# Kernel tuning notes

Measured on AMD Instinct MI355X. Metric: run time of the kernel, lower is better.

The kernel has to match this reference:

```python
import jax, jax.numpy as jnp
import numpy as np

B, T = 512, 200
N_SKILLS, M, DK, DV, H = 1000, 50, 64, 64, 128


def setup_inputs() -> dict:
    key = jax.random.key(0)
    ks = jax.random.split(key, 12)
    inp = {
        'skill_seq': jax.random.randint(ks[0], (B, T), 0, N_SKILLS, dtype=jnp.int32),
        'correct_seq': jax.random.randint(ks[1], (B, T), 0, 2, dtype=jnp.int32),
        'mask': jnp.ones((B, T), dtype=jnp.float32),
        'skill_embed': jax.random.normal(ks[2], (N_SKILLS, DK), dtype=jnp.float32),
        'key_memory': jax.random.normal(ks[3], (M, DK), dtype=jnp.float32) * 0.1,
        'value_init': jnp.zeros((M, DV), dtype=jnp.float32),
        'interaction_embed': jax.random.normal(ks[4], (2 * N_SKILLS, DV), dtype=jnp.float32),
        'erase_W': jax.random.normal(ks[5], (DV, DV), dtype=jnp.float32) * 0.05,
        'erase_b': jnp.zeros((DV,), dtype=jnp.float32),
        'add_W': jax.random.normal(ks[6], (DV, DV), dtype=jnp.float32) * 0.05,
        'add_b': jnp.zeros((DV,), dtype=jnp.float32),
        'fc1_W': jax.random.normal(ks[7], (DK + DV, H), dtype=jnp.float32) * 0.05,
        'fc1_b': jnp.zeros((H,), dtype=jnp.float32),
        'fc2_W': jax.random.normal(ks[8], (H, 1), dtype=jnp.float32) * 0.05,
        'fc2_b': jnp.zeros((1,), dtype=jnp.float32),
    }
    return inp


def reference(skill_seq, correct_seq, mask, skill_embed, key_memory, value_init,
              interaction_embed, erase_W, erase_b, add_W, add_b,
              fc1_W, fc1_b, fc2_W, fc2_b):
    n_skills = skill_embed.shape[0]
    b = skill_seq.shape[0]
    # Time-invariant-per-step quantities are precomputed vectorized over (B,T):
    q = skill_embed[skill_seq]                                   # (B,T,dk)
    w = jax.nn.softmax(jnp.einsum('btk,mk->btm', q, key_memory), axis=-1)  # (B,T,M)
    v = interaction_embed[skill_seq + correct_seq * n_skills]    # (B,T,dv)
    e = jax.nn.sigmoid(v @ erase_W + erase_b)                    # (B,T,dv)
    a = jnp.tanh(v @ add_W + add_b)                              # (B,T,dv)

    def step(mem, inputs):
        # mem: (B,M,dv); read BEFORE write, matching the torch loop
        w_t, e_t, a_t = inputs                                   # (B,M),(B,dv),(B,dv)
        read = jnp.einsum('bm,bmv->bv', w_t, mem)                # (B,dv)
        we = w_t[:, :, None]                                     # (B,M,1)
        mem = mem * (1.0 - we * e_t[:, None, :]) + we * a_t[:, None, :]
        return mem, read

    mem0 = jnp.broadcast_to(value_init, (b,) + value_init.shape)
    _, reads = jax.lax.scan(step, mem0,
                            (jnp.swapaxes(w, 0, 1), jnp.swapaxes(e, 0, 1), jnp.swapaxes(a, 0, 1)))
    reads = jnp.swapaxes(reads, 0, 1)                            # (B,T,dv)

    x = jnp.concatenate([q, reads], axis=-1)                     # (B,T,dk+dv)
    h = jax.nn.relu(x @ fc1_W + fc1_b)
    logit = (h @ fc2_W + fc2_b)[..., 0]
    p = jax.nn.sigmoid(logit)
    return p * mask, correct_seq.astype(jnp.float32) * mask
```

## Files before the change

kernel.cpp:

```cpp
#include <hip/hip_runtime.h>
#include <hip/hip_bf16.h>

#define B_  512
#define T_  200
#define NS  1000
#define M_  50
#define DK  64
#define DV  64
#define H_  128
#define NPOS (B_ * T_)

typedef __hip_bfloat16 bf16;
typedef unsigned short ushort_t;
typedef __bf16 bf16x8 __attribute__((ext_vector_type(8)));
typedef float  f32x4  __attribute__((ext_vector_type(4)));

__device__ __forceinline__ float ldf(const void* p, int i, int isbf) {
    return isbf ? __bfloat162float(((const bf16*)p)[i]) : ((const float*)p)[i];
}
__device__ __forceinline__ int sniff(const void* mask) {
    return (*(const unsigned*)mask == 0x3F800000u) ? 0 : 1;
}
__device__ __forceinline__ float rl(float x, int l) {
    return __int_as_float(__builtin_amdgcn_readlane(__float_as_int(x), l));
}
__device__ __forceinline__ ushort_t f2bf(float v) {
    bf16 h = __float2bfloat16(v);
    return *(ushort_t*)&h;
}

__global__ __launch_bounds__(256) void dk27_tabs(
    const void* __restrict__ mask,
    const void* __restrict__ skill_embed, const void* __restrict__ key_memory,
    const void* __restrict__ inter,
    const void* __restrict__ eW, const void* __restrict__ eb,
    const void* __restrict__ aW, const void* __restrict__ ab,
    const void* __restrict__ fc1W, const void* __restrict__ fc1b,
    float* __restrict__ w_tab, unsigned* __restrict__ ea_tab,
    float* __restrict__ hq2, ushort_t* __restrict__ W2f) {
    int isbf = sniff(mask);
    int lane = threadIdx.x & 63;
    int gwid = (blockIdx.x << 2) | (threadIdx.x >> 6);

    if (gwid < NS) {
        int s = gwid;
        float q = ldf(skill_embed, s * DK + lane, isbf);
        float acc = 0.f;
        if (lane < M_) {
            #pragma unroll 16
            for (int k = 0; k < DK; ++k)
                acc = fmaf(rl(q, k), ldf(key_memory, lane * DK + k, isbf), acc);
        }
        float val = (lane < M_) ? acc : -1e30f;
        float mx = val;
        #pragma unroll
        for (int off = 1; off < 64; off <<= 1) mx = fmaxf(mx, __shfl_xor(mx, off, 64));
        float ex = (lane < M_) ? __expf(val - mx) : 0.f;
        float sm = ex;
        #pragma unroll
        for (int off = 1; off < 64; off <<= 1) sm += __shfl_xor(sm, off, 64);
        w_tab[s * 64 + lane] = (lane < M_) ? ex / sm : 0.f;
    } else if (gwid < 3 * NS) {
        int r = gwid - NS;
        float vv = ldf(inter, r * DV + lane, isbf);
        float eacc = ldf(eb, lane, isbf);
        float aacc = ldf(ab, lane, isbf);
        #pragma unroll 16
        for (int u = 0; u < DV; ++u) {
            float vu = rl(vv, u);
            eacc = fmaf(vu, ldf(eW, u * DV + lane, isbf), eacc);
            aacc = fmaf(vu, ldf(aW, u * DV + lane, isbf), aacc);
        }
        float ev = 1.f / (1.f + __expf(-eacc));
        float av = tanhf(aacc);
        ea_tab[r * 64 + lane] = ((unsigned)f2bf(av) << 16) | (unsigned)f2bf(ev);
    } else if (gwid < 4 * NS) {
        int s = gwid - 3 * NS;
        float q = ldf(skill_embed, s * DK + lane, isbf);
        float acc0 = ldf(fc1b, lane, isbf);
        float acc1 = ldf(fc1b, 64 + lane, isbf);
        #pragma unroll 16
        for (int k = 0; k < DK; ++k) {
            float qk = rl(q, k);
            acc0 = fmaf(qk, ldf(fc1W, k * H_ + lane, isbf), acc0);
            acc1 = fmaf(qk, ldf(fc1W, k * H_ + 64 + lane, isbf), acc1);
        }
        hq2[s * H_ + (lane & 15) * 8 +     (lane >> 4)] = acc0;
        hq2[s * H_ + (lane & 15) * 8 + 4 + (lane >> 4)] = acc1;
    } else if (gwid < 4 * NS + 16) {
        int f = gwid - 4 * NS;
        int tile = f >> 1, kk = f & 1;
        int n = tile * 16 + (lane & 15);
        #pragma unroll
        for (int j = 0; j < 8; ++j) {
            int v = kk * 32 + (lane >> 4) * 8 + j;
            W2f[(f * 64 + lane) * 8 + j] = f2bf(ldf(fc1W, (DK + v) * H_ + n, isbf));
        }
    }
}


#define SCROW(W, MEM) \
    acc0 = fmaf(W.x, MEM.x, acc0); \
    acc1 = fmaf(W.y, MEM.y, acc1); \
    acc2 = fmaf(W.z, MEM.z, acc2); \
    acc3 = fmaf(W.w, MEM.w, acc3); \
    MEM.x = fmaf(-W.x, fmaf(e0, MEM.x, -a0), MEM.x); \
    MEM.y = fmaf(-W.y, fmaf(e0, MEM.y, -a0), MEM.y); \
    MEM.z = fmaf(-W.z, fmaf(e0, MEM.z, -a0), MEM.z); \
    MEM.w = fmaf(-W.w, fmaf(e0, MEM.w, -a0), MEM.w);

#define VPTR(P) { size_t u_ = (size_t)(P); asm volatile("" : "+v"(u_)); \
                  (P) = (const f32x4*)u_; }

#define REFILL(ST, S, C) { \
    const f32x4* p_ = (const f32x4*)w_tab + (S) * 16 + 4 * k; \
    VPTR(p_) \
    w##ST##0 = p_[0]; w##ST##1 = p_[1]; w##ST##2 = p_[2]; w##ST##3 = p_[3]; \
    ea##ST = ea_tab[((S) + (C) * NS) * 64 + lane]; }

#define STEP(ST, TP) { \
    float e0 = __uint_as_float(ea##ST << 16); \
    float a0 = __uint_as_float(ea##ST & 0xFFFF0000u); \
    float acc0 = 0.f, acc1 = 0.f, acc2 = 0.f, acc3 = 0.f; \
    SCROW(w##ST##0, mem[0]) SCROW(w##ST##1, mem[1]) \
    SCROW(w##ST##2, mem[2]) SCROW(w##ST##3, mem[3]) \
    read_bf[outb + (TP) * 256] = f2bf((acc0 + acc1) + (acc2 + acc3)); \
    REFILL(ST, curS[TP], curC[TP]) }

__global__ __launch_bounds__(64, 2) void dk27_scan(
    const int*  __restrict__ ss, const int* __restrict__ cs,
    const void* __restrict__ mask, const void* __restrict__ value_init,
    const float* __restrict__ w_tab, const unsigned* __restrict__ ea_tab,
    ushort_t* __restrict__ read_bf) {

    int isbf = sniff(mask);
    int lane = threadIdx.x;
    int bk   = blockIdx.x;
    int b    = bk >> 2, k = bk & 3;
    const int base = b * T_;

    float4 mem[4];
    #pragma unroll
    for (int i = 0; i < 4; ++i) {
        int r = 16 * k + 4 * i;
        mem[i].x = (r + 0 < M_) ? ldf(value_init, (r + 0) * DV + lane, isbf) : 0.f;
        mem[i].y = (r + 1 < M_) ? ldf(value_init, (r + 1) * DV + lane, isbf) : 0.f;
        mem[i].z = (r + 2 < M_) ? ldf(value_init, (r + 2) * DV + lane, isbf) : 0.f;
        mem[i].w = (r + 3 < M_) ? ldf(value_init, (r + 3) * DV + lane, isbf) : 0.f;
    }

    int curS[8], curC[8], nxtS[8], nxtC[8];
    #pragma unroll
    for (int j = 0; j < 8; ++j) { nxtS[j] = ss[base + 2 + j]; nxtC[j] = cs[base + 2 + j]; }

    f32x4 wA0, wA1, wA2, wA3, wB0, wB1, wB2, wB3;
    unsigned eaA, eaB;
    {
        int s_ = ss[base + 0], c_ = cs[base + 0];
        REFILL(A, s_, c_)
        s_ = ss[base + 1]; c_ = cs[base + 1];
        REFILL(B, s_, c_)
    }

    size_t outb = ((size_t)base * 4 + k) * 64 + lane;

    for (int cc = 0; cc < 25; ++cc) {
        #pragma unroll
        for (int j = 0; j < 8; ++j) { curS[j] = nxtS[j]; curC[j] = nxtC[j]; }
        int tb = 8 * cc + 10;
        #pragma unroll
        for (int j = 0; j < 8; ++j) {
            int tf = tb + j; tf = tf < T_ ? tf : T_ - 1;
            nxtS[j] = ss[base + tf]; nxtC[j] = cs[base + tf];
        }
        STEP(A, 0) STEP(B, 1) STEP(A, 2) STEP(B, 3)
        STEP(A, 4) STEP(B, 5) STEP(A, 6) STEP(B, 7)
        outb += 2048;
    }
}

#define FOR8(X) X(0) X(1) X(2) X(3) X(4) X(5) X(6) X(7)
#define DECL_C(t)  f32x4 c##t = {0.f, 0.f, 0.f, 0.f};
#define LOADB(t) bf16x8 b##t##_0 = B8[(2 * (t)) * 64 + lane], \
                        b##t##_1 = B8[(2 * (t) + 1) * 64 + lane];
#define FCKK(kk, p) { \
    bf16x8 av = A8[col * 32 + (kk) * 4 + quad]; \
    c0 = __builtin_amdgcn_mfma_f32_16x16x32_bf16(av, b0_##p, c0, 0, 0, 0); \
    c1 = __builtin_amdgcn_mfma_f32_16x16x32_bf16(av, b1_##p, c1, 0, 0, 0); \
    c2 = __builtin_amdgcn_mfma_f32_16x16x32_bf16(av, b2_##p, c2, 0, 0, 0); \
    c3 = __builtin_amdgcn_mfma_f32_16x16x32_bf16(av, b3_##p, c3, 0, 0, 0); \
    c4 = __builtin_amdgcn_mfma_f32_16x16x32_bf16(av, b4_##p, c4, 0, 0, 0); \
    c5 = __builtin_amdgcn_mfma_f32_16x16x32_bf16(av, b5_##p, c5, 0, 0, 0); \
    c6 = __builtin_amdgcn_mfma_f32_16x16x32_bf16(av, b6_##p, c6, 0, 0, 0); \
    c7 = __builtin_amdgcn_mfma_f32_16x16x32_bf16(av, b7_##p, c7, 0, 0, 0); }
#define HQ(r, t) (((t) < 4) ? qa##r[(t) & 3] : qb##r[(t) & 3])
#define EPI(t) { \
    float h; \
    h = c##t.x + HQ(0, t); x0 = fmaf(fmaxf(h, 0.f), f2w##t, x0); \
    h = c##t.y + HQ(1, t); x1 = fmaf(fmaxf(h, 0.f), f2w##t, x1); \
    h = c##t.z + HQ(2, t); x2 = fmaf(fmaxf(h, 0.f), f2w##t, x2); \
    h = c##t.w + HQ(3, t); x3 = fmaf(fmaxf(h, 0.f), f2w##t, x3); }

__global__ __launch_bounds__(64)
__attribute__((amdgpu_waves_per_eu(3))) void dk27_fc(
    const int*  __restrict__ skill_seq, const int* __restrict__ correct_seq,
    const void* __restrict__ mask,
    const void* __restrict__ fc2W, const void* __restrict__ fc2b,
    const float* __restrict__ hq2, const ushort_t* __restrict__ W2f,
    const ushort_t* __restrict__ read_bf,
    float* __restrict__ out0, float* __restrict__ out1) {

    int isbf = sniff(mask);
    int lane = threadIdx.x;
    int col  = lane & 15, quad = lane >> 4;

    const bf16x8* B8 = (const bf16x8*)W2f;
    FOR8(LOADB)

    float f2w0 = ldf(fc2W,   0 + col, isbf), f2w1 = ldf(fc2W,  16 + col, isbf);
    float f2w2 = ldf(fc2W,  32 + col, isbf), f2w3 = ldf(fc2W,  48 + col, isbf);
    float f2w4 = ldf(fc2W,  64 + col, isbf), f2w5 = ldf(fc2W,  80 + col, isbf);
    float f2w6 = ldf(fc2W,  96 + col, isbf), f2w7 = ldf(fc2W, 112 + col, isbf);
    float f2b  = ldf(fc2b, 0, isbf);

    for (int pg = blockIdx.x; pg < NPOS / 16; pg += gridDim.x) {
        int p0 = pg * 16;
        const bf16x8* A8 = (const bf16x8*)(read_bf + (size_t)p0 * 256);

        int s0r = skill_seq[p0 + quad * 4 + 0];
        int s1r = skill_seq[p0 + quad * 4 + 1];
        int s2r = skill_seq[p0 + quad * 4 + 2];
        int s3r = skill_seq[p0 + quad * 4 + 3];

        f32x4 qa0 = *(const f32x4*)(hq2 + s0r * H_ + col * 8);
        f32x4 qb0 = *(const f32x4*)(hq2 + s0r * H_ + col * 8 + 4);
        f32x4 qa1 = *(const f32x4*)(hq2 + s1r * H_ + col * 8);
        f32x4 qb1 = *(const f32x4*)(hq2 + s1r * H_ + col * 8 + 4);
        f32x4 qa2 = *(const f32x4*)(hq2 + s2r * H_ + col * 8);
        f32x4 qb2 = *(const f32x4*)(hq2 + s2r * H_ + col * 8 + 4);
        f32x4 qa3 = *(const f32x4*)(hq2 + s3r * H_ + col * 8);
        f32x4 qb3 = *(const f32x4*)(hq2 + s3r * H_ + col * 8 + 4);

        FOR8(DECL_C)
        FCKK(0, 0) FCKK(1, 1) FCKK(2, 0) FCKK(3, 1)
        FCKK(4, 0) FCKK(5, 1) FCKK(6, 0) FCKK(7, 1)

        float x0 = 0.f, x1 = 0.f, x2 = 0.f, x3 = 0.f;
        FOR8(EPI)

        #pragma unroll
        for (int off = 1; off < 16; off <<= 1) {
            x0 += __shfl_xor(x0, off, 64);
            x1 += __shfl_xor(x1, off, 64);
            x2 += __shfl_xor(x2, off, 64);
            x3 += __shfl_xor(x3, off, 64);
        }

        float mk0 = ldf(mask, p0 + quad * 4 + 0, isbf);
        float mk1 = ldf(mask, p0 + quad * 4 + 1, isbf);
        float mk2 = ldf(mask, p0 + quad * 4 + 2, isbf);
        float mk3 = ldf(mask, p0 + quad * 4 + 3, isbf);
        if (col == 0) {
            out0[p0 + quad * 4 + 0] = mk0 / (1.f + __expf(-(x0 + f2b)));
            out0[p0 + quad * 4 + 1] = mk1 / (1.f + __expf(-(x1 + f2b)));
            out0[p0 + quad * 4 + 2] = mk2 / (1.f + __expf(-(x2 + f2b)));
            out0[p0 + quad * 4 + 3] = mk3 / (1.f + __expf(-(x3 + f2b)));
        }
        if (col == 1) {
            out1[p0 + quad * 4 + 0] = (float)correct_seq[p0 + quad * 4 + 0] * mk0;
            out1[p0 + quad * 4 + 1] = (float)correct_seq[p0 + quad * 4 + 1] * mk1;
            out1[p0 + quad * 4 + 2] = (float)correct_seq[p0 + quad * 4 + 2] * mk2;
            out1[p0 + quad * 4 + 3] = (float)correct_seq[p0 + quad * 4 + 3] * mk3;
        }
    }
}

extern "C" void kernel_launch(void* const* d_in, const int* in_sizes, int n_in,
                              void* d_out, int out_size, void* d_ws, size_t ws_size,
                              hipStream_t stream) {
    const int*  skill_seq   = (const int*)d_in[0];
    const int*  correct_seq = (const int*)d_in[1];
    const void* mask        = d_in[2];
    const void* skill_embed = d_in[3];
    const void* key_memory  = d_in[4];
    const void* value_init  = d_in[5];
    const void* inter       = d_in[6];
    const void* erase_W     = d_in[7];
    const void* erase_b     = d_in[8];
    const void* add_W       = d_in[9];
    const void* add_b       = d_in[10];
    const void* fc1_W       = d_in[11];
    const void* fc1_b       = d_in[12];
    const void* fc2_W       = d_in[13];
    const void* fc2_b       = d_in[14];
    float* out = (float*)d_out;

    float*    ws      = (float*)d_ws + 16;
    float*    w_tab   = ws;
    unsigned* ea_tab  = (unsigned*)(ws + 64000);
    float*    hq2     = ws + 192000;
    ushort_t* W2f     = (ushort_t*)(ws + 320000);
    ushort_t* read_bf = (ushort_t*)(ws + 336400);

    dk27_tabs<<<1004, 256, 0, stream>>>(mask, skill_embed, key_memory, inter,
                                        erase_W, erase_b, add_W, add_b,
                                        fc1_W, fc1_b,
                                        w_tab, ea_tab, hq2, W2f);

    dk27_scan<<<B_ * 4, 64, 0, stream>>>(skill_seq, correct_seq, mask, value_init,
                                         w_tab, ea_tab, read_bf);

    dk27_fc<<<3200, 64, 0, stream>>>(skill_seq, correct_seq, mask,
                                     fc2_W, fc2_b, hq2, W2f, read_bf,
                                     out, out + (size_t)NPOS);
}
```

Measured before the change: 197.8 us.

## Precompute combined interaction index and restructure scan prefetch with sched barriers

```diff
diff --git a/kernel.cpp b/kernel.cpp
--- a/kernel.cpp
+++ b/kernel.cpp
@@ -29,7 +29,8 @@
     return *(ushort_t*)&h;
 }
 
-__global__ __launch_bounds__(256) void dk27_tabs(
+__global__ __launch_bounds__(256) void dk28_tabs(
+    const int*  __restrict__ ss, const int* __restrict__ cs,
     const void* __restrict__ mask,
     const void* __restrict__ skill_embed, const void* __restrict__ key_memory,
     const void* __restrict__ inter,
@@ -37,7 +38,8 @@
     const void* __restrict__ aW, const void* __restrict__ ab,
     const void* __restrict__ fc1W, const void* __restrict__ fc1b,
     float* __restrict__ w_tab, unsigned* __restrict__ ea_tab,
-    float* __restrict__ hq2, ushort_t* __restrict__ W2f) {
+    float* __restrict__ hq2, ushort_t* __restrict__ W2f,
+    int* __restrict__ qix) {
     int isbf = sniff(mask);
     int lane = threadIdx.x & 63;
     int gwid = (blockIdx.x << 2) | (threadIdx.x >> 6);
@@ -96,40 +98,74 @@
             int v = kk * 32 + (lane >> 4) * 8 + j;
             W2f[(f * 64 + lane) * 8 + j] = f2bf(ldf(fc1W, (DK + v) * H_ + n, isbf));
         }
+    } else if (gwid < 4 * NS + 16 + 400) {
+        int qp = gwid - (4 * NS + 16);
+        int t0 = qp * 256;
+        #pragma unroll
+        for (int i = 0; i < 4; ++i) {
+            int idx = t0 + i * 64 + lane;
+            qix[idx] = ss[idx] + cs[idx] * NS;
+        }
     }
 }
 
 
-#define SCROW(W, MEM) \
-    acc0 = fmaf(W.x, MEM.x, acc0); \
-    acc1 = fmaf(W.y, MEM.y, acc1); \
-    acc2 = fmaf(W.z, MEM.z, acc2); \
-    acc3 = fmaf(W.w, MEM.w, acc3); \
-    MEM.x = fmaf(-W.x, fmaf(e0, MEM.x, -a0), MEM.x); \
-    MEM.y = fmaf(-W.y, fmaf(e0, MEM.y, -a0), MEM.y); \
-    MEM.z = fmaf(-W.z, fmaf(e0, MEM.z, -a0), MEM.z); \
-    MEM.w = fmaf(-W.w, fmaf(e0, MEM.w, -a0), MEM.w);
-
-#define VPTR(P) { size_t u_ = (size_t)(P); asm volatile("" : "+v"(u_)); \
-                  (P) = (const f32x4*)u_; }
-
-#define REFILL(ST, S, C) { \
-    const f32x4* p_ = (const f32x4*)w_tab + (S) * 16 + 4 * k; \
-    VPTR(p_) \
-    w##ST##0 = p_[0]; w##ST##1 = p_[1]; w##ST##2 = p_[2]; w##ST##3 = p_[3]; \
-    ea##ST = ea_tab[((S) + (C) * NS) * 64 + lane]; }
-
-#define STEP(ST, TP) { \
-    float e0 = __uint_as_float(ea##ST << 16); \
-    float a0 = __uint_as_float(ea##ST & 0xFFFF0000u); \
+#define SB0 __builtin_amdgcn_sched_barrier(0);
+
+#define SCROW1(WV, MM, ACC) \
+    ACC = fmaf(WV, MM, ACC); \
+    MM = fmaf(-(WV), fmaf(e0, MM, -a0), MM);
+
+#define SC_STEP(D, EAR, TP, QR) { \
+    float e0 = __uint_as_float(EAR << 16); \
+    float a0 = __uint_as_float(EAR & 0xFFFF0000u); \
     float acc0 = 0.f, acc1 = 0.f, acc2 = 0.f, acc3 = 0.f; \
-    SCROW(w##ST##0, mem[0]) SCROW(w##ST##1, mem[1]) \
-    SCROW(w##ST##2, mem[2]) SCROW(w##ST##3, mem[3]) \
+    SCROW1(D[0],  mem[0].x, acc0) SCROW1(D[1],  mem[0].y, acc1) \
+    SCROW1(D[2],  mem[0].z, acc2) SCROW1(D[3],  mem[0].w, acc3) \
+    SCROW1(D[4],  mem[1].x, acc0) SCROW1(D[5],  mem[1].y, acc1) \
+    SCROW1(D[6],  mem[1].z, acc2) SCROW1(D[7],  mem[1].w, acc3) \
+    SCROW1(D[8],  mem[2].x, acc0) SCROW1(D[9],  mem[2].y, acc1) \
+    SCROW1(D[10], mem[2].z, acc2) SCROW1(D[11], mem[2].w, acc3) \
+    SCROW1(D[12], mem[3].x, acc0) SCROW1(D[13], mem[3].y, acc1) \
+    SCROW1(D[14], mem[3].z, acc2) SCROW1(D[15], mem[3].w, acc3) \
     read_bf[outb + (TP) * 256] = f2bf((acc0 + acc1) + (acc2 + acc3)); \
-    REFILL(ST, curS[TP], curC[TP]) }
-
-__global__ __launch_bounds__(64, 2) void dk27_scan(
-    const int*  __restrict__ ss, const int* __restrict__ cs,
+    EAR = ea_tab[(unsigned)(QR) * 64 + lane]; \
+}
+
+#define FILL_W(D, Q) { \
+    int s_ = (Q) < NS ? (Q) : (Q) - NS; \
+    const float* wp_ = w_tab + s_ * 64 + 16 * k; \
+    _Pragma("unroll") \
+    for (int z = 0; z < 16; ++z) D[z] = wp_[z]; \
+}
+
+#define LDQ(QF, J, TBN) { \
+    int t_ = (TBN) + (J); t_ = t_ < T_ ? t_ : T_ - 1; \
+    QF[J] = qix[base + t_]; \
+}
+
+#define CHUNK(QC, QF, TBN) { \
+    SC_STEP(wA0, eaA, 0, QC[2]) \
+    SB0 FILL_W(wB0, QC[2]) FILL_W(wB1, QC[3]) \
+        LDQ(QF, 0, TBN) LDQ(QF, 1, TBN) SB0 \
+    SC_STEP(wA1, eaB, 1, QC[3]) \
+    SC_STEP(wB0, eaA, 2, QC[4]) \
+    SB0 FILL_W(wA0, QC[4]) FILL_W(wA1, QC[5]) \
+        LDQ(QF, 2, TBN) LDQ(QF, 3, TBN) SB0 \
+    SC_STEP(wB1, eaB, 3, QC[5]) \
+    SC_STEP(wA0, eaA, 4, QC[6]) \
+    SB0 FILL_W(wB0, QC[6]) FILL_W(wB1, QC[7]) \
+        LDQ(QF, 4, TBN) LDQ(QF, 5, TBN) SB0 \
+    SC_STEP(wA1, eaB, 5, QC[7]) \
+    SC_STEP(wB0, eaA, 6, QF[0]) \
+    SB0 FILL_W(wA0, QF[0]) FILL_W(wA1, QF[1]) \
+        LDQ(QF, 6, TBN) LDQ(QF, 7, TBN) SB0 \
+    SC_STEP(wB1, eaB, 7, QF[1]) \
+    outb += 2048; \
+}
+
+__global__ __launch_bounds__(64, 2) void dk28_scan(
+    const int*  __restrict__ qix,
     const void* __restrict__ mask, const void* __restrict__ value_init,
     const float* __restrict__ w_tab, const unsigned* __restrict__ ea_tab,
     ushort_t* __restrict__ read_bf) {
@@ -150,34 +186,26 @@
         mem[i].w = (r + 3 < M_) ? ldf(value_init, (r + 3) * DV + lane, isbf) : 0.f;
     }
 
-    int curS[8], curC[8], nxtS[8], nxtC[8];
+    int qA[8], qN[8];
     #pragma unroll
-    for (int j = 0; j < 8; ++j) { nxtS[j] = ss[base + 2 + j]; nxtC[j] = cs[base + 2 + j]; }
-
-    f32x4 wA0, wA1, wA2, wA3, wB0, wB1, wB2, wB3;
+    for (int j = 0; j < 8; ++j) qA[j] = qix[base + j];
+
+    float wA0[16], wA1[16], wB0[16], wB1[16];
     unsigned eaA, eaB;
-    {
-        int s_ = ss[base + 0], c_ = cs[base + 0];
-        REFILL(A, s_, c_)
-        s_ = ss[base + 1]; c_ = cs[base + 1];
-        REFILL(B, s_, c_)
+    FILL_W(wA0, qA[0])
+    FILL_W(wA1, qA[1])
+    eaA = ea_tab[(unsigned)qA[0] * 64 + lane];
+    eaB = ea_tab[(unsigned)qA[1] * 64 + lane];
+
+    size_t outb = ((size_t)base * 4 + k) * 64 + lane;
+
+    int tb = 8;
+    for (int cc2 = 0; cc2 < 12; ++cc2) {
+        CHUNK(qA, qN, tb)
+        CHUNK(qN, qA, tb + 8)
+        tb += 16;
     }
-
-    size_t outb = ((size_t)base * 4 + k) * 64 + lane;
-
-    for (int cc = 0; cc < 25; ++cc) {
-        #pragma unroll
-        for (int j = 0; j < 8; ++j) { curS[j] = nxtS[j]; curC[j] = nxtC[j]; }
-        int tb = 8 * cc + 10;
-        #pragma unroll
-        for (int j = 0; j < 8; ++j) {
-            int tf = tb + j; tf = tf < T_ ? tf : T_ - 1;
-            nxtS[j] = ss[base + tf]; nxtC[j] = cs[base + tf];
-        }
-        STEP(A, 0) STEP(B, 1) STEP(A, 2) STEP(B, 3)
-        STEP(A, 4) STEP(B, 5) STEP(A, 6) STEP(B, 7)
-        outb += 2048;
-    }
+    CHUNK(qA, qN, 200)
 }
 
 #define FOR8(X) X(0) X(1) X(2) X(3) X(4) X(5) X(6) X(7)
@@ -203,7 +231,7 @@
     h = c##t.w + HQ(3, t); x3 = fmaf(fmaxf(h, 0.f), f2w##t, x3); }
 
 __global__ __launch_bounds__(64)
-__attribute__((amdgpu_waves_per_eu(3))) void dk27_fc(
+__attribute__((amdgpu_waves_per_eu(3))) void dk28_fc(
     const int*  __restrict__ skill_seq, const int* __restrict__ correct_seq,
     const void* __restrict__ mask,
     const void* __restrict__ fc2W, const void* __restrict__ fc2b,
@@ -302,16 +330,18 @@
     float*    hq2     = ws + 192000;
     ushort_t* W2f     = (ushort_t*)(ws + 320000);
     ushort_t* read_bf = (ushort_t*)(ws + 336400);
-
-    dk27_tabs<<<1004, 256, 0, stream>>>(mask, skill_embed, key_memory, inter,
+    int*      qix     = (int*)(out + (size_t)NPOS);
+
+    dk28_tabs<<<1104, 256, 0, stream>>>(skill_seq, correct_seq,
+                                        mask, skill_embed, key_memory, inter,
                                         erase_W, erase_b, add_W, add_b,
                                         fc1_W, fc1_b,
-                                        w_tab, ea_tab, hq2, W2f);
-
-    dk27_scan<<<B_ * 4, 64, 0, stream>>>(skill_seq, correct_seq, mask, value_init,
+                                        w_tab, ea_tab, hq2, W2f, qix);
+
+    dk28_scan<<<B_ * 4, 64, 0, stream>>>(qix, mask, value_init,
                                          w_tab, ea_tab, read_bf);
 
-    dk27_fc<<<3200, 64, 0, stream>>>(skill_seq, correct_seq, mask,
+    dk28_fc<<<3200, 64, 0, stream>>>(skill_seq, correct_seq, mask,
                                      fc2_W, fc2_b, hq2, W2f, read_bf,
                                      out, out + (size_t)NPOS);
 }
```

Result: no change. 199.7 us (+1.0%).

## Fuse memory scan with FC head per sequence, staging reads in LDS

Applied to the files above, without the earlier changes.

```diff
diff --git a/kernel.cpp b/kernel.cpp
--- a/kernel.cpp
+++ b/kernel.cpp
@@ -29,7 +29,8 @@
     return *(ushort_t*)&h;
 }
 
-__global__ __launch_bounds__(256) void dk27_tabs(
+__global__ __launch_bounds__(256) void dk30_tabs(
+    const int*  __restrict__ cseq,
     const void* __restrict__ mask,
     const void* __restrict__ skill_embed, const void* __restrict__ key_memory,
     const void* __restrict__ inter,
@@ -37,7 +38,8 @@
     const void* __restrict__ aW, const void* __restrict__ ab,
     const void* __restrict__ fc1W, const void* __restrict__ fc1b,
     float* __restrict__ w_tab, unsigned* __restrict__ ea_tab,
-    float* __restrict__ hq2, ushort_t* __restrict__ W2f) {
+    float* __restrict__ hq2, ushort_t* __restrict__ W2f,
+    float* __restrict__ out1) {
     int isbf = sniff(mask);
     int lane = threadIdx.x & 63;
     int gwid = (blockIdx.x << 2) | (threadIdx.x >> 6);
@@ -96,11 +98,19 @@
             int v = kk * 32 + (lane >> 4) * 8 + j;
             W2f[(f * 64 + lane) * 8 + j] = f2bf(ldf(fc1W, (DK + v) * H_ + n, isbf));
         }
+    } else if (gwid < 4 * NS + 16 + 400) {
+        int qp = gwid - (4 * NS + 16);
+        int t0 = qp * 256;
+        #pragma unroll
+        for (int i = 0; i < 4; ++i) {
+            int idx = t0 + i * 64 + lane;
+            out1[idx] = (float)cseq[idx] * ldf(mask, idx, isbf);
+        }
     }
 }
 
 
-#define SCROW(W, MEM) \
+#define FSCROW(W, MEM) \
     acc0 = fmaf(W.x, MEM.x, acc0); \
     acc1 = fmaf(W.y, MEM.y, acc1); \
     acc2 = fmaf(W.z, MEM.z, acc2); \
@@ -110,35 +120,49 @@
     MEM.z = fmaf(-W.z, fmaf(e0, MEM.z, -a0), MEM.z); \
     MEM.w = fmaf(-W.w, fmaf(e0, MEM.w, -a0), MEM.w);
 
-#define VPTR(P) { size_t u_ = (size_t)(P); asm volatile("" : "+v"(u_)); \
-                  (P) = (const f32x4*)u_; }
-
-#define REFILL(ST, S, C) { \
-    const f32x4* p_ = (const f32x4*)w_tab + (S) * 16 + 4 * k; \
-    VPTR(p_) \
-    w##ST##0 = p_[0]; w##ST##1 = p_[1]; w##ST##2 = p_[2]; w##ST##3 = p_[3]; \
-    ea##ST = ea_tab[((S) + (C) * NS) * 64 + lane]; }
-
-#define STEP(ST, TP) { \
-    float e0 = __uint_as_float(ea##ST << 16); \
-    float a0 = __uint_as_float(ea##ST & 0xFFFF0000u); \
+#define FSTEP(EAR, WARR, TP, TT) { \
+    float e0 = __uint_as_float(EAR << 16); \
+    float a0 = __uint_as_float(EAR & 0xFFFF0000u); \
     float acc0 = 0.f, acc1 = 0.f, acc2 = 0.f, acc3 = 0.f; \
-    SCROW(w##ST##0, mem[0]) SCROW(w##ST##1, mem[1]) \
-    SCROW(w##ST##2, mem[2]) SCROW(w##ST##3, mem[3]) \
-    read_bf[outb + (TP) * 256] = f2bf((acc0 + acc1) + (acc2 + acc3)); \
-    REFILL(ST, curS[TP], curC[TP]) }
-
-__global__ __launch_bounds__(64, 2) void dk27_scan(
+    FSCROW(WARR[0], mem[0]) FSCROW(WARR[1], mem[1]) \
+    FSCROW(WARR[2], mem[2]) FSCROW(WARR[3], mem[3]) \
+    rb[buf][TP][(k << 6) | lane] = f2bf((acc0 + acc1) + (acc2 + acc3)); \
+    EAR = ea_tab[(s2 + c2 * NS) * 64 + lane]; \
+    WARR[0] = w4[s2 * 16 + 4 * k + 0]; \
+    WARR[1] = w4[s2 * 16 + 4 * k + 1]; \
+    WARR[2] = w4[s2 * 16 + 4 * k + 2]; \
+    WARR[3] = w4[s2 * 16 + 4 * k + 3]; \
+    s2 = s3; c2 = c3; \
+    { int tf = (TT) + 4; tf = tf < T_ ? tf : T_ - 1; \
+      s3 = ss[base + tf]; c3 = cs[base + tf]; } }
+
+__global__ __launch_bounds__(256, 2) void dk30_fused(
     const int*  __restrict__ ss, const int* __restrict__ cs,
     const void* __restrict__ mask, const void* __restrict__ value_init,
     const float* __restrict__ w_tab, const unsigned* __restrict__ ea_tab,
-    ushort_t* __restrict__ read_bf) {
+    const float* __restrict__ hq2, const ushort_t* __restrict__ W2f,
+    const void* __restrict__ fc2W, const void* __restrict__ fc2b,
+    float* __restrict__ out0) {
+
+    __shared__ ushort_t rb[2][16][256];
+    __shared__ float    xs[4][16];
 
     int isbf = sniff(mask);
-    int lane = threadIdx.x;
-    int bk   = blockIdx.x;
-    int b    = bk >> 2, k = bk & 3;
+    int lane = threadIdx.x & 63;
+    int k    = threadIdx.x >> 6;
+    int b    = blockIdx.x;
     const int base = b * T_;
+    const float4* w4 = (const float4*)w_tab;
+    int col = lane & 15, quad = lane >> 4;
+
+    const bf16x8* B8 = (const bf16x8*)W2f;
+    bf16x8 bA0 = B8[(2 * (2 * k)    ) * 64 + lane];
+    bf16x8 bA1 = B8[(2 * (2 * k) + 1) * 64 + lane];
+    bf16x8 bB0 = B8[(2 * (2 * k + 1)    ) * 64 + lane];
+    bf16x8 bB1 = B8[(2 * (2 * k + 1) + 1) * 64 + lane];
+    float f2wA = ldf(fc2W, (2 * k)     * 16 + col, isbf);
+    float f2wB = ldf(fc2W, (2 * k + 1) * 16 + col, isbf);
+    float f2b  = ldf(fc2b, 0, isbf);
 
     float4 mem[4];
     #pragma unroll
@@ -150,128 +174,90 @@
         mem[i].w = (r + 3 < M_) ? ldf(value_init, (r + 3) * DV + lane, isbf) : 0.f;
     }
 
-    int curS[8], curC[8], nxtS[8], nxtC[8];
-    #pragma unroll
-    for (int j = 0; j < 8; ++j) { nxtS[j] = ss[base + 2 + j]; nxtC[j] = cs[base + 2 + j]; }
-
-    f32x4 wA0, wA1, wA2, wA3, wB0, wB1, wB2, wB3;
+    int s2 = ss[base + 2], c2 = cs[base + 2];
+    int s3 = ss[base + 3], c3 = cs[base + 3];
+
+    float4 wa[4], wb[4];
     unsigned eaA, eaB;
     {
-        int s_ = ss[base + 0], c_ = cs[base + 0];
-        REFILL(A, s_, c_)
-        s_ = ss[base + 1]; c_ = cs[base + 1];
-        REFILL(B, s_, c_)
+        int sA = ss[base], cA = cs[base];
+        eaA = ea_tab[(sA + cA * NS) * 64 + lane];
+        #pragma unroll
+        for (int i = 0; i < 4; ++i) wa[i] = w4[sA * 16 + 4 * k + i];
+        int sB = ss[base + 1], cB = cs[base + 1];
+        eaB = ea_tab[(sB + cB * NS) * 64 + lane];
+        #pragma unroll
+        for (int i = 0; i < 4; ++i) wb[i] = w4[sB * 16 + 4 * k + i];
     }
 
-    size_t outb = ((size_t)base * 4 + k) * 64 + lane;
-
-    for (int cc = 0; cc < 25; ++cc) {
-        #pragma unroll
-        for (int j = 0; j < 8; ++j) { curS[j] = nxtS[j]; curC[j] = nxtC[j]; }
-        int tb = 8 * cc + 10;
-        #pragma unroll
-        for (int j = 0; j < 8; ++j) {
-            int tf = tb + j; tf = tf < T_ ? tf : T_ - 1;
-            nxtS[j] = ss[base + tf]; nxtC[j] = cs[base + tf];
-        }
-        STEP(A, 0) STEP(B, 1) STEP(A, 2) STEP(B, 3)
-        STEP(A, 4) STEP(B, 5) STEP(A, 6) STEP(B, 7)
-        outb += 2048;
-    }
-}
-
-#define FOR8(X) X(0) X(1) X(2) X(3) X(4) X(5) X(6) X(7)
-#define DECL_C(t)  f32x4 c##t = {0.f, 0.f, 0.f, 0.f};
-#define LOADB(t) bf16x8 b##t##_0 = B8[(2 * (t)) * 64 + lane], \
-                        b##t##_1 = B8[(2 * (t) + 1) * 64 + lane];
-#define FCKK(kk, p) { \
-    bf16x8 av = A8[col * 32 + (kk) * 4 + quad]; \
-    c0 = __builtin_amdgcn_mfma_f32_16x16x32_bf16(av, b0_##p, c0, 0, 0, 0); \
-    c1 = __builtin_amdgcn_mfma_f32_16x16x32_bf16(av, b1_##p, c1, 0, 0, 0); \
-    c2 = __builtin_amdgcn_mfma_f32_16x16x32_bf16(av, b2_##p, c2, 0, 0, 0); \
-    c3 = __builtin_amdgcn_mfma_f32_16x16x32_bf16(av, b3_##p, c3, 0, 0, 0); \
-    c4 = __builtin_amdgcn_mfma_f32_16x16x32_bf16(av, b4_##p, c4, 0, 0, 0); \
-    c5 = __builtin_amdgcn_mfma_f32_16x16x32_bf16(av, b5_##p, c5, 0, 0, 0); \
-    c6 = __builtin_amdgcn_mfma_f32_16x16x32_bf16(av, b6_##p, c6, 0, 0, 0); \
-    c7 = __builtin_amdgcn_mfma_f32_16x16x32_bf16(av, b7_##p, c7, 0, 0, 0); }
-#define HQ(r, t) (((t) < 4) ? qa##r[(t) & 3] : qb##r[(t) & 3])
-#define EPI(t) { \
-    float h; \
-    h = c##t.x + HQ(0, t); x0 = fmaf(fmaxf(h, 0.f), f2w##t, x0); \
-    h = c##t.y + HQ(1, t); x1 = fmaf(fmaxf(h, 0.f), f2w##t, x1); \
-    h = c##t.z + HQ(2, t); x2 = fmaf(fmaxf(h, 0.f), f2w##t, x2); \
-    h = c##t.w + HQ(3, t); x3 = fmaf(fmaxf(h, 0.f), f2w##t, x3); }
-
-__global__ __launch_bounds__(64)
-__attribute__((amdgpu_waves_per_eu(3))) void dk27_fc(
-    const int*  __restrict__ skill_seq, const int* __restrict__ correct_seq,
-    const void* __restrict__ mask,
-    const void* __restrict__ fc2W, const void* __restrict__ fc2b,
-    const float* __restrict__ hq2, const ushort_t* __restrict__ W2f,
-    const ushort_t* __restrict__ read_bf,
-    float* __restrict__ out0, float* __restrict__ out1) {
-
-    int isbf = sniff(mask);
-    int lane = threadIdx.x;
-    int col  = lane & 15, quad = lane >> 4;
-
-    const bf16x8* B8 = (const bf16x8*)W2f;
-    FOR8(LOADB)
-
-    float f2w0 = ldf(fc2W,   0 + col, isbf), f2w1 = ldf(fc2W,  16 + col, isbf);
-    float f2w2 = ldf(fc2W,  32 + col, isbf), f2w3 = ldf(fc2W,  48 + col, isbf);
-    float f2w4 = ldf(fc2W,  64 + col, isbf), f2w5 = ldf(fc2W,  80 + col, isbf);
-    float f2w6 = ldf(fc2W,  96 + col, isbf), f2w7 = ldf(fc2W, 112 + col, isbf);
-    float f2b  = ldf(fc2b, 0, isbf);
-
-    for (int pg = blockIdx.x; pg < NPOS / 16; pg += gridDim.x) {
-        int p0 = pg * 16;
-        const bf16x8* A8 = (const bf16x8*)(read_bf + (size_t)p0 * 256);
-
-        int s0r = skill_seq[p0 + quad * 4 + 0];
-        int s1r = skill_seq[p0 + quad * 4 + 1];
-        int s2r = skill_seq[p0 + quad * 4 + 2];
-        int s3r = skill_seq[p0 + quad * 4 + 3];
-
-        f32x4 qa0 = *(const f32x4*)(hq2 + s0r * H_ + col * 8);
-        f32x4 qb0 = *(const f32x4*)(hq2 + s0r * H_ + col * 8 + 4);
-        f32x4 qa1 = *(const f32x4*)(hq2 + s1r * H_ + col * 8);
-        f32x4 qb1 = *(const f32x4*)(hq2 + s1r * H_ + col * 8 + 4);
-        f32x4 qa2 = *(const f32x4*)(hq2 + s2r * H_ + col * 8);
-        f32x4 qb2 = *(const f32x4*)(hq2 + s2r * H_ + col * 8 + 4);
-        f32x4 qa3 = *(const f32x4*)(hq2 + s3r * H_ + col * 8);
-        f32x4 qb3 = *(const f32x4*)(hq2 + s3r * H_ + col * 8 + 4);
-
-        FOR8(DECL_C)
-        FCKK(0, 0) FCKK(1, 1) FCKK(2, 0) FCKK(3, 1)
-        FCKK(4, 0) FCKK(5, 1) FCKK(6, 0) FCKK(7, 1)
-
-        float x0 = 0.f, x1 = 0.f, x2 = 0.f, x3 = 0.f;
-        FOR8(EPI)
-
-        #pragma unroll
-        for (int off = 1; off < 16; off <<= 1) {
-            x0 += __shfl_xor(x0, off, 64);
-            x1 += __shfl_xor(x1, off, 64);
-            x2 += __shfl_xor(x2, off, 64);
-            x3 += __shfl_xor(x3, off, 64);
-        }
-
-        float mk0 = ldf(mask, p0 + quad * 4 + 0, isbf);
-        float mk1 = ldf(mask, p0 + quad * 4 + 1, isbf);
-        float mk2 = ldf(mask, p0 + quad * 4 + 2, isbf);
-        float mk3 = ldf(mask, p0 + quad * 4 + 3, isbf);
-        if (col == 0) {
-            out0[p0 + quad * 4 + 0] = mk0 / (1.f + __expf(-(x0 + f2b)));
-            out0[p0 + quad * 4 + 1] = mk1 / (1.f + __expf(-(x1 + f2b)));
-            out0[p0 + quad * 4 + 2] = mk2 / (1.f + __expf(-(x2 + f2b)));
-            out0[p0 + quad * 4 + 3] = mk3 / (1.f + __expf(-(x3 + f2b)));
-        }
-        if (col == 1) {
-            out1[p0 + quad * 4 + 0] = (float)correct_seq[p0 + quad * 4 + 0] * mk0;
-            out1[p0 + quad * 4 + 1] = (float)correct_seq[p0 + quad * 4 + 1] * mk1;
-            out1[p0 + quad * 4 + 2] = (float)correct_seq[p0 + quad * 4 + 2] * mk2;
-            out1[p0 + quad * 4 + 3] = (float)correct_seq[p0 + quad * 4 + 3] * mk3;
+    for (int cc = 0; cc < 13; ++cc) {
+        int buf   = cc & 1;
+        int p0    = cc * 16;
+        int nstep = (cc == 12) ? 8 : 16;
+
+        for (int tp = 0; tp < nstep; tp += 2) {
+            int t = p0 + tp;
+            FSTEP(eaA, wa, tp,     t)
+            FSTEP(eaB, wb, tp + 1, t + 1)
+        }
+        __syncthreads();
+
+        {
+            int pA = p0 + quad * 4;
+            int i0 = pA + 0 < T_ ? pA + 0 : T_ - 1;
+            int i1 = pA + 1 < T_ ? pA + 1 : T_ - 1;
+            int i2 = pA + 2 < T_ ? pA + 2 : T_ - 1;
+            int i3 = pA + 3 < T_ ? pA + 3 : T_ - 1;
+            int sp0 = ss[base + i0], sp1 = ss[base + i1];
+            int sp2 = ss[base + i2], sp3 = ss[base + i3];
+            float2 h0 = *(const float2*)(hq2 + sp0 * H_ + col * 8 + 2 * k);
+            float2 h1 = *(const float2*)(hq2 + sp1 * H_ + col * 8 + 2 * k);
+            float2 h2 = *(const float2*)(hq2 + sp2 * H_ + col * 8 + 2 * k);
+            float2 h3 = *(const float2*)(hq2 + sp3 * H_ + col * 8 + 2 * k);
+
+            f32x4 cA = {0.f, 0.f, 0.f, 0.f}, cB = {0.f, 0.f, 0.f, 0.f};
+            const bf16x8* A8 = (const bf16x8*)&rb[buf][0][0];
+            #pragma unroll
+            for (int kk = 0; kk < 8; ++kk) {
+                bf16x8 av = A8[col * 32 + kk * 4 + quad];
+                if (kk & 1) {
+                    cA = __builtin_amdgcn_mfma_f32_16x16x32_bf16(av, bA1, cA, 0, 0, 0);
+                    cB = __builtin_amdgcn_mfma_f32_16x16x32_bf16(av, bB1, cB, 0, 0, 0);
+                } else {
+                    cA = __builtin_amdgcn_mfma_f32_16x16x32_bf16(av, bA0, cA, 0, 0, 0);
+                    cB = __builtin_amdgcn_mfma_f32_16x16x32_bf16(av, bB0, cB, 0, 0, 0);
+                }
+            }
+            float x0, x1, x2, x3, h;
+            h = cA.x + h0.x; x0  = fmaxf(h, 0.f) * f2wA;
+            h = cB.x + h0.y; x0 += fmaxf(h, 0.f) * f2wB;
+            h = cA.y + h1.x; x1  = fmaxf(h, 0.f) * f2wA;
+            h = cB.y + h1.y; x1 += fmaxf(h, 0.f) * f2wB;
+            h = cA.z + h2.x; x2  = fmaxf(h, 0.f) * f2wA;
+            h = cB.z + h2.y; x2 += fmaxf(h, 0.f) * f2wB;
+            h = cA.w + h3.x; x3  = fmaxf(h, 0.f) * f2wA;
+            h = cB.w + h3.y; x3 += fmaxf(h, 0.f) * f2wB;
+            #pragma unroll
+            for (int off = 1; off < 16; off <<= 1) {
+                x0 += __shfl_xor(x0, off, 64);
+                x1 += __shfl_xor(x1, off, 64);
+                x2 += __shfl_xor(x2, off, 64);
+                x3 += __shfl_xor(x3, off, 64);
+            }
+            if (col == 0) {
+                xs[k][quad * 4 + 0] = x0;
+                xs[k][quad * 4 + 1] = x1;
+                xs[k][quad * 4 + 2] = x2;
+                xs[k][quad * 4 + 3] = x3;
+            }
+        }
+        __syncthreads();
+
+        if (k == 0 && lane < 16 && p0 + lane < T_) {
+            int p = base + p0 + lane;
+            float xsum = xs[0][lane] + xs[1][lane] + xs[2][lane] + xs[3][lane] + f2b;
+            float mk = ldf(mask, p, isbf);
+            out0[p] = mk / (1.f + __expf(-xsum));
         }
     }
 }
@@ -301,17 +287,14 @@
     unsigned* ea_tab  = (unsigned*)(ws + 64000);
     float*    hq2     = ws + 192000;
     ushort_t* W2f     = (ushort_t*)(ws + 320000);
-    ushort_t* read_bf = (ushort_t*)(ws + 336400);
-
-    dk27_tabs<<<1004, 256, 0, stream>>>(mask, skill_embed, key_memory, inter,
-                                        erase_W, erase_b, add_W, add_b,
+
+    dk30_tabs<<<1104, 256, 0, stream>>>(correct_seq, mask, skill_embed, key_memory,
+                                        inter, erase_W, erase_b, add_W, add_b,
                                         fc1_W, fc1_b,
-                                        w_tab, ea_tab, hq2, W2f);
-
-    dk27_scan<<<B_ * 4, 64, 0, stream>>>(skill_seq, correct_seq, mask, value_init,
-                                         w_tab, ea_tab, read_bf);
-
-    dk27_fc<<<3200, 64, 0, stream>>>(skill_seq, correct_seq, mask,
-                                     fc2_W, fc2_b, hq2, W2f, read_bf,
-                                     out, out + (size_t)NPOS);
-}
+                                        w_tab, ea_tab, hq2, W2f,
+                                        out + (size_t)NPOS);
+
+    dk30_fused<<<B_, 256, 0, stream>>>(skill_seq, correct_seq, mask, value_init,
+                                       w_tab, ea_tab, hq2, W2f, fc2_W, fc2_b,
+                                       out);
+}
```

New measurement: 167.5 us. -15.3%, faster.
